# Kernel optimization log

Measured on AMD Instinct MI355X. Metric: run time of the kernel, lower is better.

The kernel has to match this reference:

```python
import math
import jax, jax.numpy as jnp
import numpy as np

B, L, D, H, V, R, NL = 4, 1024, 1024, 16, 50257, 4, 3
LORA_SCALE = 32.0 / R  # alpha / r
EPS = 1e-5
GELU_C = math.sqrt(2.0 / math.pi)


def gelu(x):
    return 0.5 * x * (1.0 + jnp.tanh(GELU_C * (x + 0.044715 * x ** 3)))


def layer_norm(x, w, b):
    u = x.mean(-1, keepdims=True)
    s = ((x - u) ** 2).mean(-1, keepdims=True)
    return w * (x - u) / jnp.sqrt(s + EPS) + b


def setup_inputs() -> dict:
    key = jax.random.key(0)
    ks = jax.random.split(key, 10)
    std = 0.02
    inp = {
        'input_ids': jax.random.randint(ks[0], (B, L), 0, V),
        'wte': jax.random.normal(ks[1], (V, D), jnp.float32) * std,
        'wpe': jax.random.normal(ks[2], (L, D), jnp.float32) * std,
        'ln1_w': jnp.ones((NL, D), jnp.float32),
        'ln1_b': jnp.zeros((NL, D), jnp.float32),
        'attn_w': jax.random.normal(ks[3], (NL, D, 3 * D), jnp.float32) * std,
        'attn_b': jnp.zeros((NL, 3 * D), jnp.float32),
        'lora_A': jax.random.normal(ks[4], (NL, 2 * R, D), jnp.float32) * std,
        'lora_B': jax.random.normal(ks[5], (NL, 2 * D, R), jnp.float32) * std,
        'proj_w': jax.random.normal(ks[6], (NL, D, D), jnp.float32) * std,
        'proj_b': jnp.zeros((NL, D), jnp.float32),
        'ln2_w': jnp.ones((NL, D), jnp.float32),
        'ln2_b': jnp.zeros((NL, D), jnp.float32),
        'fc_w': jax.random.normal(ks[7], (NL, D, 4 * D), jnp.float32) * std,
        'fc_b': jnp.zeros((NL, 4 * D), jnp.float32),
        'fc2_w': jax.random.normal(ks[8], (NL, 4 * D, D), jnp.float32) * std,
        'fc2_b': jnp.zeros((NL, D), jnp.float32),
    }
    return inp


def block(x, causal, p):
    (ln1w, ln1b, aw, ab, lA, lB, pw, pb, ln2w, ln2b, fw, fb, f2w, f2b) = p
    h = layer_norm(x, ln1w, ln1b)
    # LoRA-merged QKV: base GEMM + low-rank deltas on Q and V groups
    qkv = h @ aw + ab                     # [B,L,3D]
    after_A = h @ lA.T                    # [B,L,2R]
    dq = after_A[..., :R] @ lB[:D].T * LORA_SCALE   # [B,L,D]
    dv = after_A[..., R:] @ lB[D:].T * LORA_SCALE   # [B,L,D]
    q = qkv[..., :D] + dq
    k = qkv[..., D:2 * D]
    v = qkv[..., 2 * D:] + dv
    # split heads -> [B,H,L,hd]
    hd = D // H
    q = q.reshape(B, L, H, hd).transpose(0, 2, 1, 3)
    k = k.reshape(B, L, H, hd).transpose(0, 2, 1, 3)
    v = v.reshape(B, L, H, hd).transpose(0, 2, 1, 3)
    w = jnp.einsum('bhqd,bhkd->bhqk', q, k) / math.sqrt(hd)
    w = w * causal - 1e10 * (1.0 - causal)  # multiplicative causal mask trick
    w = jax.nn.softmax(w, axis=-1)
    a = jnp.einsum('bhqk,bhkd->bhqd', w, v)
    a = a.transpose(0, 2, 1, 3).reshape(B, L, D)
    a = a @ pw + pb
    x = x + a
    m = layer_norm(x, ln2w, ln2b)
    m = gelu(m @ fw + fb) @ f2w + f2b
    return x + m


def reference(input_ids, wte, wpe, ln1_w, ln1_b, attn_w, attn_b, lora_A, lora_B,
              proj_w, proj_b, ln2_w, ln2_b, fc_w, fc_b, fc2_w, fc2_b):
    pos = jnp.arange(L)
    x = wte[input_ids] + wpe[pos][None, :, :]   # [B,L,D]
    causal = jnp.tril(jnp.ones((L, L), x.dtype))
    for i in range(NL):
        p = (ln1_w[i], ln1_b[i], attn_w[i], attn_b[i], lora_A[i], lora_B[i],
             proj_w[i], proj_b[i], ln2_w[i], ln2_b[i], fc_w[i], fc_b[i],
             fc2_w[i], fc2_b[i])
        x = block(x, causal, p)
    return x
```

## Files before the change

kernel.cpp:

```cpp
#include <hip/hip_runtime.h>

typedef __bf16 bf16x8 __attribute__((ext_vector_type(8)));
typedef float f32x4 __attribute__((ext_vector_type(4)));
typedef unsigned short u16x8 __attribute__((ext_vector_type(8)));
typedef unsigned short u16x4 __attribute__((ext_vector_type(4)));

#define DEV static __device__ __forceinline__

DEV unsigned short f2bf(float f){
  unsigned int u = __builtin_bit_cast(unsigned int, f);
  u += 0x7fffu + ((u >> 16) & 1u);
  return (unsigned short)(u >> 16);
}
DEV float bf2f(unsigned short h){
  return __builtin_bit_cast(float, ((unsigned int)h) << 16);
}
DEV f32x4 bf4_to_f32(u16x4 h){
  f32x4 r = {bf2f(h[0]), bf2f(h[1]), bf2f(h[2]), bf2f(h[3])};
  return r;
}
DEV float gelu_f(float x){
  float z = 0.7978845608028654f * (x + 0.044715f * x * x * x);
  float e = __expf(2.0f * z);
  float th = 1.0f - 2.0f / (e + 1.0f);
  return 0.5f * x * (1.0f + th);
}

#define BAR() do{ asm volatile("" ::: "memory"); __builtin_amdgcn_s_barrier(); asm volatile("" ::: "memory"); }while(0)
#define LGKM0() asm volatile("s_waitcnt lgkmcnt(0)" ::: "memory")

__global__ __launch_bounds__(256)
void prep_weights(const float* __restrict__ attnw, const float* __restrict__ lorA,
                  const float* __restrict__ lorB, const float* __restrict__ projw,
                  const float* __restrict__ fcw, const float* __restrict__ fc2w,
                  unsigned short* __restrict__ WTA, unsigned short* __restrict__ WTP,
                  unsigned short* __restrict__ WTF, unsigned short* __restrict__ WTF2){
  __shared__ float tile[32][33];
  const int blk = blockIdx.x;
  const int layer = blk / 12288;
  const int r = blk % 12288;
  const float* in; unsigned short* out; int R, C, bx, by; bool lora;
  if (r < 3072){
    in = attnw + (size_t)layer*1024*3072; out = WTA + (size_t)layer*3072*1024;
    R = 1024; C = 3072; bx = r % 96; by = r / 96; lora = true;
  } else if (r < 4096){
    int rr = r - 3072;
    in = projw + (size_t)layer*1024*1024; out = WTP + (size_t)layer*1024*1024;
    R = 1024; C = 1024; bx = rr % 32; by = rr / 32; lora = false;
  } else if (r < 8192){
    int rr = r - 4096;
    in = fcw + (size_t)layer*1024*4096; out = WTF + (size_t)layer*4096*1024;
    R = 1024; C = 4096; bx = rr % 128; by = rr / 128; lora = false;
  } else {
    int rr = r - 8192;
    in = fc2w + (size_t)layer*4096*1024; out = WTF2 + (size_t)layer*1024*4096;
    R = 4096; C = 1024; bx = rr % 32; by = rr / 32; lora = false;
  }
  const int tx = threadIdx.x & 31, ty = threadIdx.x >> 5;
  const int r0 = by * 32, c0 = bx * 32;
  #pragma unroll
  for (int k = 0; k < 4; ++k)
    tile[ty + k*8][tx] = in[(size_t)(r0 + ty + k*8) * C + c0 + tx];
  float la0=0.f, la1=0.f, la2=0.f, la3=0.f;
  int seg = 0;
  if (lora){
    const float* lA = lorA + (size_t)layer*8192;
    seg = (c0 < 1024) ? 0 : ((c0 >= 2048) ? 2 : 1);
    if (seg != 1){
      const int kk = r0 + tx;
      const int rb = (seg == 0) ? 0 : 4;
      la0 = lA[(rb+0)*1024 + kk]; la1 = lA[(rb+1)*1024 + kk];
      la2 = lA[(rb+2)*1024 + kk]; la3 = lA[(rb+3)*1024 + kk];
    }
  }
  __syncthreads();
  const float* lB = lorB + (size_t)layer*8192;
  #pragma unroll
  for (int k = 0; k < 4; ++k){
    int rr = ty + k*8;
    int c = c0 + rr;
    float v = tile[tx][rr];
    if (lora && seg != 1){
      int lbrow = (seg == 0) ? c : (c - 1024);
      f32x4 lb = *(const f32x4*)(lB + (size_t)lbrow*4);
      v += 8.0f * (la0*lb[0] + la1*lb[1] + la2*lb[2] + la3*lb[3]);
    }
    if (lora && seg == 1) v *= 0.125f;
    out[(size_t)c * R + r0 + tx] = f2bf(v);
  }
}

DEV void ln_finish(f32x4 v, const float* __restrict__ wgt,
                   const float* __restrict__ bia, unsigned short* __restrict__ out,
                   int m, int t, float* red){
  float s  = v[0] + v[1] + v[2] + v[3];
  float ss = v[0]*v[0] + v[1]*v[1] + v[2]*v[2] + v[3]*v[3];
  #pragma unroll
  for (int off = 32; off >= 1; off >>= 1){
    s  += __shfl_xor(s, off);
    ss += __shfl_xor(ss, off);
  }
  if ((t & 63) == 0){ red[(t>>6)*2] = s; red[(t>>6)*2+1] = ss; }
  __syncthreads();
  float S  = red[0] + red[2] + red[4] + red[6];
  float SS = red[1] + red[3] + red[5] + red[7];
  float mean = S * (1.0f/1024.0f);
  float var  = SS * (1.0f/1024.0f) - mean*mean;
  float rstd = rsqrtf(var + 1e-5f);
  f32x4 wv = *(const f32x4*)(wgt + t*4);
  f32x4 bv = *(const f32x4*)(bia + t*4);
  u16x4 o;
  #pragma unroll
  for (int j = 0; j < 4; ++j) o[j] = f2bf(wv[j] * (v[j] - mean) * rstd + bv[j]);
  *(u16x4*)(out + (size_t)m * 1024 + t*4) = o;
}

__global__ __launch_bounds__(256)
void embed_ln(const int* __restrict__ ids, const float* __restrict__ wte,
              const float* __restrict__ wpe, const float* __restrict__ wgt,
              const float* __restrict__ bia, float* __restrict__ x,
              unsigned short* __restrict__ hb){
  __shared__ float red[8];
  const int m = blockIdx.x, t = threadIdx.x;
  const int id = ids[m], lpos = m & 1023;
  f32x4 a = *(const f32x4*)(wte + (size_t)id * 1024 + t*4);
  f32x4 p = *(const f32x4*)(wpe + (size_t)lpos * 1024 + t*4);
  f32x4 v = a + p;
  *(f32x4*)(x + (size_t)m * 1024 + t*4) = v;
  ln_finish(v, wgt, bia, hb, m, t, red);
}

__global__ __launch_bounds__(256)
void ln_kernel(const float* __restrict__ x, const float* __restrict__ wgt,
               const float* __restrict__ bia, unsigned short* __restrict__ out){
  __shared__ float red[8];
  const int m = blockIdx.x, t = threadIdx.x;
  f32x4 v = *(const f32x4*)(x + (size_t)m * 1024 + t*4);
  ln_finish(v, wgt, bia, out, m, t, red);
}

__global__ __launch_bounds__(256)
void reduce_ln(const unsigned short* __restrict__ P, const float* __restrict__ res,
               const float* __restrict__ bias, float* __restrict__ xout,
               const float* __restrict__ wgt, const float* __restrict__ bia,
               unsigned short* __restrict__ hb){
  __shared__ float red[8];
  const int m = blockIdx.x, t = threadIdx.x;
  const size_t off = (size_t)m*1024 + t*4;
  const size_t MN = (size_t)4096*1024;
  f32x4 v = bf4_to_f32(*(const u16x4*)(P + off));
  v += bf4_to_f32(*(const u16x4*)(P + MN + off));
  v += bf4_to_f32(*(const u16x4*)(P + 2*MN + off));
  v += bf4_to_f32(*(const u16x4*)(P + 3*MN + off));
  v += *(const f32x4*)(res + off);
  v += *(const f32x4*)(bias + t*4);
  *(f32x4*)(xout + off) = v;
  ln_finish(v, wgt, bia, hb, m, t, red);
}

__global__ __launch_bounds__(256)
void fc2_reduce(const unsigned short* __restrict__ P, const float* __restrict__ res,
                const float* __restrict__ bias, float* __restrict__ out){
  const int m = blockIdx.x, t = threadIdx.x;
  const size_t off = (size_t)m*1024 + t*4;
  const size_t MN = (size_t)4096*1024;
  f32x4 v = bf4_to_f32(*(const u16x4*)(P + off));
  v += bf4_to_f32(*(const u16x4*)(P + MN + off));
  v += bf4_to_f32(*(const u16x4*)(P + 2*MN + off));
  v += bf4_to_f32(*(const u16x4*)(P + 3*MN + off));
  v += *(const f32x4*)(res + off);
  v += *(const f32x4*)(bias + t*4);
  *(f32x4*)(out + off) = v;
}

__global__ __launch_bounds__(256)
void assemble_vt(const unsigned short* __restrict__ qkv,
                 unsigned short* __restrict__ Vto){
  __shared__ unsigned short vt[64 * 72];
  const int t = threadIdx.x;
  const int bh = blockIdx.y, b = bh >> 4, h = bh & 15;
  const int l0 = blockIdx.x * 64;
  {
    const int li = t >> 2, c0 = (t & 3) * 16;
    const unsigned short* src = qkv + (size_t)(b*1024 + l0 + li)*3072 + 2048 + h*64 + c0;
    u16x8 v0 = *(const u16x8*)(src);
    u16x8 v1 = *(const u16x8*)(src + 8);
    #pragma unroll
    for (int j = 0; j < 8; ++j){
      vt[(c0 + j)*72 + li]     = v0[j];
      vt[(c0 + 8 + j)*72 + li] = v1[j];
    }
  }
  __syncthreads();
  {
    const int dh = t >> 2, lc = (t & 3) * 16;
    u16x8 lo = *(const u16x8*)(&vt[dh*72 + lc]);
    u16x8 hi = *(const u16x8*)(&vt[dh*72 + lc + 8]);
    unsigned short* dst = Vto + ((size_t)(bh*64 + dh)) * 1024 + l0 + lc;
    *(u16x8*)(dst)     = lo;
    *(u16x8*)(dst + 8) = hi;
  }
}

template<int MODE>
__global__ __launch_bounds__(512, 1)
void gemm256(const unsigned short* __restrict__ A,
             const unsigned short* __restrict__ Wt,
             const float* __restrict__ bias,
             void* __restrict__ outp, int M, int N, int K, int ldk){
  extern __shared__ char sm[];
  const int t = threadIdx.x, w = t >> 6, l = t & 63, g = l >> 4, q = l & 15;
  const int wr = w >> 2, wc = w & 3;
  const int gx = gridDim.x;
  const int nwg = gx * gridDim.y;
  const int id  = blockIdx.x + gx * blockIdx.y;
  const int id2 = (id & 7) * (nwg >> 3) + (id >> 3);
  const int bm = (id2 / gx) * 256, bn = (id2 % gx) * 256;
  const int koff = blockIdx.z * K;
  const int NT = K >> 6;
  const int sr = t >> 3, sc = (t & 7) ^ (sr & 7);
  __attribute__((address_space(3))) char* smAS = (__attribute__((address_space(3))) char*)sm;

#define STAGE_A(slot, qd, tile) do{ \
    const unsigned short* _s = A + (size_t)(bm + (qd)*64 + sr)*ldk + koff + ((tile)<<6) + sc*8; \
    __builtin_amdgcn_global_load_lds((const __attribute__((address_space(1))) void*)_s, \
      (__attribute__((address_space(3))) void*)(smAS + (slot)*32768 + (qd)*8192 + t*16), 16, 0, 0); }while(0)
#define STAGE_B(slot, qd, tile) do{ \
    const unsigned short* _s = Wt + (size_t)(bn + (qd)*64 + sr)*ldk + koff + ((tile)<<6) + sc*8; \
    __builtin_amdgcn_global_load_lds((const __attribute__((address_space(1))) void*)_s, \
      (__attribute__((address_space(3))) void*)(smAS + 65536 + (slot)*32768 + (qd)*8192 + t*16), 16, 0, 0); }while(0)

  const int arow = (wr*128 + q) * 128;
  const int brow = (wc*64  + q) * 128;
  const int c0 = ((g    ) ^ (q & 7)) << 4;
  const int c1 = ((4 + g) ^ (q & 7)) << 4;

  f32x4 acc[8][4];
  #pragma unroll
  for (int m = 0; m < 8; ++m)
    #pragma unroll
    for (int n = 0; n < 4; ++n) acc[m][n] = (f32x4){0.f,0.f,0.f,0.f};

  STAGE_A(0,0,0); STAGE_A(0,1,0); STAGE_A(0,2,0); STAGE_A(0,3,0);
  STAGE_B(0,0,0); STAGE_B(0,1,0); STAGE_B(0,2,0); STAGE_B(0,3,0);
  if (NT > 1){
    STAGE_B(1,0,1); STAGE_B(1,1,1); STAGE_B(1,2,1); STAGE_B(1,3,1);
    STAGE_A(1,0,1); STAGE_A(1,2,1);
    asm volatile("s_waitcnt vmcnt(6)" ::: "memory");
  } else {
    asm volatile("s_waitcnt vmcnt(0)" ::: "memory");
  }
  BAR();

  u16x8 bk0[4], bk1[4];
  for (int T = 0; T < NT; ++T){
    const int cur = T & 1, nxt = cur ^ 1;
    const int curA = cur*32768, curB = 65536 + cur*32768;
    if (T + 1 < NT){ STAGE_A(nxt, 1, T+1); STAGE_A(nxt, 3, T+1); }
    u16x8 a00 = *(const u16x8*)(sm + curA + arow + 0*2048 + c0);
    u16x8 a01 = *(const u16x8*)(sm + curA + arow + 0*2048 + c1);
    u16x8 a10 = *(const u16x8*)(sm + curA + arow + 1*2048 + c0);
    u16x8 a11 = *(const u16x8*)(sm + curA + arow + 1*2048 + c1);
    #pragma unroll
    for (int n = 0; n < 4; ++n){
      bk0[n] = *(const u16x8*)(sm + curB + brow + n*2048 + c0);
      bk1[n] = *(const u16x8*)(sm + curB + brow + n*2048 + c1);
    }
    BAR(); LGKM0();
    __builtin_amdgcn_s_setprio(1);
    #pragma unroll
    for (int n = 0; n < 4; ++n){
      acc[0][n] = __builtin_amdgcn_mfma_f32_16x16x32_bf16(__builtin_bit_cast(bf16x8,a00), __builtin_bit_cast(bf16x8,bk0[n]), acc[0][n], 0,0,0);
      acc[0][n] = __builtin_amdgcn_mfma_f32_16x16x32_bf16(__builtin_bit_cast(bf16x8,a01), __builtin_bit_cast(bf16x8,bk1[n]), acc[0][n], 0,0,0);
      acc[1][n] = __builtin_amdgcn_mfma_f32_16x16x32_bf16(__builtin_bit_cast(bf16x8,a10), __builtin_bit_cast(bf16x8,bk0[n]), acc[1][n], 0,0,0);
      acc[1][n] = __builtin_amdgcn_mfma_f32_16x16x32_bf16(__builtin_bit_cast(bf16x8,a11), __builtin_bit_cast(bf16x8,bk1[n]), acc[1][n], 0,0,0);
    }
    __builtin_amdgcn_s_setprio(0);
    BAR();
    if (T + 2 < NT){ STAGE_B(cur, 0, T+2); STAGE_B(cur, 1, T+2); }
    a00 = *(const u16x8*)(sm + curA + arow + 2*2048 + c0);
    a01 = *(const u16x8*)(sm + curA + arow + 2*2048 + c1);
    a10 = *(const u16x8*)(sm + curA + arow + 3*2048 + c0);
    a11 = *(const u16x8*)(sm + curA + arow + 3*2048 + c1);
    BAR(); LGKM0();
    __builtin_amdgcn_s_setprio(1);
    #pragma unroll
    for (int n = 0; n < 4; ++n){
      acc[2][n] = __builtin_amdgcn_mfma_f32_16x16x32_bf16(__builtin_bit_cast(bf16x8,a00), __builtin_bit_cast(bf16x8,bk0[n]), acc[2][n], 0,0,0);
      acc[2][n] = __builtin_amdgcn_mfma_f32_16x16x32_bf16(__builtin_bit_cast(bf16x8,a01), __builtin_bit_cast(bf16x8,bk1[n]), acc[2][n], 0,0,0);
      acc[3][n] = __builtin_amdgcn_mfma_f32_16x16x32_bf16(__builtin_bit_cast(bf16x8,a10), __builtin_bit_cast(bf16x8,bk0[n]), acc[3][n], 0,0,0);
      acc[3][n] = __builtin_amdgcn_mfma_f32_16x16x32_bf16(__builtin_bit_cast(bf16x8,a11), __builtin_bit_cast(bf16x8,bk1[n]), acc[3][n], 0,0,0);
    }
    __builtin_amdgcn_s_setprio(0);
    BAR();
    if (T + 2 < NT){ STAGE_B(cur, 2, T+2); STAGE_B(cur, 3, T+2); STAGE_A(cur, 0, T+2); STAGE_A(cur, 2, T+2); }
    a00 = *(const u16x8*)(sm + curA + arow + 4*2048 + c0);
    a01 = *(const u16x8*)(sm + curA + arow + 4*2048 + c1);
    a10 = *(const u16x8*)(sm + curA + arow + 5*2048 + c0);
    a11 = *(const u16x8*)(sm + curA + arow + 5*2048 + c1);
    BAR(); LGKM0();
    __builtin_amdgcn_s_setprio(1);
    #pragma unroll
    for (int n = 0; n < 4; ++n){
      acc[4][n] = __builtin_amdgcn_mfma_f32_16x16x32_bf16(__builtin_bit_cast(bf16x8,a00), __builtin_bit_cast(bf16x8,bk0[n]), acc[4][n], 0,0,0);
      acc[4][n] = __builtin_amdgcn_mfma_f32_16x16x32_bf16(__builtin_bit_cast(bf16x8,a01), __builtin_bit_cast(bf16x8,bk1[n]), acc[4][n], 0,0,0);
      acc[5][n] = __builtin_amdgcn_mfma_f32_16x16x32_bf16(__builtin_bit_cast(bf16x8,a10), __builtin_bit_cast(bf16x8,bk0[n]), acc[5][n], 0,0,0);
      acc[5][n] = __builtin_amdgcn_mfma_f32_16x16x32_bf16(__builtin_bit_cast(bf16x8,a11), __builtin_bit_cast(bf16x8,bk1[n]), acc[5][n], 0,0,0);
    }
    __builtin_amdgcn_s_setprio(0);
    BAR();
    a00 = *(const u16x8*)(sm + curA + arow + 6*2048 + c0);
    a01 = *(const u16x8*)(sm + curA + arow + 6*2048 + c1);
    a10 = *(const u16x8*)(sm + curA + arow + 7*2048 + c0);
    a11 = *(const u16x8*)(sm + curA + arow + 7*2048 + c1);
    if (T + 2 < NT){ asm volatile("s_waitcnt vmcnt(6)" ::: "memory"); }
    else if (T + 1 < NT){ asm volatile("s_waitcnt vmcnt(0)" ::: "memory"); }
    BAR(); LGKM0();
    __builtin_amdgcn_s_setprio(1);
    #pragma unroll
    for (int n = 0; n < 4; ++n){
      acc[6][n] = __builtin_amdgcn_mfma_f32_16x16x32_bf16(__builtin_bit_cast(bf16x8,a00), __builtin_bit_cast(bf16x8,bk0[n]), acc[6][n], 0,0,0);
      acc[6][n] = __builtin_amdgcn_mfma_f32_16x16x32_bf16(__builtin_bit_cast(bf16x8,a01), __builtin_bit_cast(bf16x8,bk1[n]), acc[6][n], 0,0,0);
      acc[7][n] = __builtin_amdgcn_mfma_f32_16x16x32_bf16(__builtin_bit_cast(bf16x8,a10), __builtin_bit_cast(bf16x8,bk0[n]), acc[7][n], 0,0,0);
      acc[7][n] = __builtin_amdgcn_mfma_f32_16x16x32_bf16(__builtin_bit_cast(bf16x8,a11), __builtin_bit_cast(bf16x8,bk1[n]), acc[7][n], 0,0,0);
    }
    __builtin_amdgcn_s_setprio(0);
    BAR();
  }
#undef STAGE_A
#undef STAGE_B
  unsigned short* pout4 = (MODE == 4) ? ((unsigned short*)outp + (size_t)blockIdx.z * M * N) : nullptr;
  #pragma unroll
  for (int n = 0; n < 4; ++n){
    int col = bn + wc*64 + n*16 + q;
    float bv = (MODE == 4) ? 0.f : bias[col];
    if (MODE == 3 && (col >> 10) == 1) bv *= 0.125f;
    #pragma unroll
    for (int m = 0; m < 8; ++m){
      int row0 = bm + wr*128 + m*16 + g*4;
      #pragma unroll
      for (int r = 0; r < 4; ++r){
        float v = acc[m][n][r] + bv;
        if (MODE == 2){
          ((unsigned short*)outp)[(size_t)(row0 + r)*N + col] = f2bf(gelu_f(v));
        } else if (MODE == 3){
          ((unsigned short*)outp)[(size_t)(row0 + r)*N + col] = f2bf(v);
        } else if (MODE == 4){
          pout4[(size_t)(row0 + r)*N + col] = f2bf(v);
        }
      }
    }
  }
}

template<int MODE>
__global__ __launch_bounds__(256)
void gemm_bf16(const unsigned short* __restrict__ A,
               const unsigned short* __restrict__ Wt,
               const float* __restrict__ bias,
               const float* __restrict__ res,
               void* __restrict__ outp,
               int M, int N, int K){
  __shared__ unsigned short As[128*32];
  __shared__ unsigned short Bs[128*32];
  const int t = threadIdx.x;
  const int w = t >> 6, l = t & 63;
  const int wr = w >> 1, wc = w & 1;
  const int g = l >> 4, q = l & 15;
  const int gxn = gridDim.x;
  const int nwg = gxn * gridDim.y;
  const int bid = blockIdx.x + gxn * blockIdx.y;
  const int bid2 = ((nwg & 7) == 0) ? ((bid & 7)*(nwg >> 3) + (bid >> 3)) : bid;
  const int bm = (bid2 / gxn) * 128, bn = (bid2 % gxn) * 128;
  const int srow = t >> 2, schunk = t & 3;
  const unsigned short* Ag = A  + (size_t)(bm + srow)*K + schunk*8;
  const unsigned short* Bg = Wt + (size_t)(bn + srow)*K + schunk*8;
  const int sa0 = srow*64        + ((schunk ^ ((srow>>1)&3)) << 4);
  const int sa1 = (srow+64)*64   + ((schunk ^ (((srow+64)>>1)&3)) << 4);
  f32x4 acc[4][4];
  #pragma unroll
  for (int m = 0; m < 4; ++m)
    #pragma unroll
    for (int n = 0; n < 4; ++n) acc[m][n] = (f32x4){0.f,0.f,0.f,0.f};
  const int nk = K >> 5;
  u16x8 ra0 = *(const u16x8*)(Ag);
  u16x8 ra1 = *(const u16x8*)(Ag + (size_t)64*K);
  u16x8 rb0 = *(const u16x8*)(Bg);
  u16x8 rb1 = *(const u16x8*)(Bg + (size_t)64*K);
  for (int kt = 0; kt < nk; ++kt){
    __syncthreads();
    *(u16x8*)((char*)As + sa0) = ra0;
    *(u16x8*)((char*)As + sa1) = ra1;
    *(u16x8*)((char*)Bs + sa0) = rb0;
    *(u16x8*)((char*)Bs + sa1) = rb1;
    __syncthreads();
    if (kt + 1 < nk){
      const unsigned short* A2 = Ag + (size_t)(kt+1)*32;
      const unsigned short* B2 = Bg + (size_t)(kt+1)*32;
      ra0 = *(const u16x8*)(A2);
      ra1 = *(const u16x8*)(A2 + (size_t)64*K);
      rb0 = *(const u16x8*)(B2);
      rb1 = *(const u16x8*)(B2 + (size_t)64*K);
    }
    bf16x8 af[4], bfr[4];
    #pragma unroll
    for (int m = 0; m < 4; ++m){
      int row = wr*64 + m*16 + q;
      af[m] = __builtin_bit_cast(bf16x8,
        *(const u16x8*)((char*)As + row*64 + ((g ^ ((row>>1)&3)) << 4)));
    }
    #pragma unroll
    for (int n = 0; n < 4; ++n){
      int row = wc*64 + n*16 + q;
      bfr[n] = __builtin_bit_cast(bf16x8,
        *(const u16x8*)((char*)Bs + row*64 + ((g ^ ((row>>1)&3)) << 4)));
    }
    #pragma unroll
    for (int m = 0; m < 4; ++m)
      #pragma unroll
      for (int n = 0; n < 4; ++n)
        acc[m][n] = __builtin_amdgcn_mfma_f32_16x16x32_bf16(af[m], bfr[n], acc[m][n], 0, 0, 0);
  }
  #pragma unroll
  for (int n = 0; n < 4; ++n){
    int col = bn + wc*64 + n*16 + q;
    float bv = bias[col];
    #pragma unroll
    for (int m = 0; m < 4; ++m){
      int row0 = bm + wr*64 + m*16 + g*4;
      #pragma unroll
      for (int r = 0; r < 4; ++r){
        int row = row0 + r;
        float v = acc[m][n][r] + bv;
        if (MODE == 1) v += res[(size_t)row*N + col];
        if (MODE == 2){
          ((unsigned short*)outp)[(size_t)row*N + col] = f2bf(gelu_f(v));
        } else {
          ((float*)outp)[(size_t)row*N + col] = v;
        }
      }
    }
  }
}

__global__ __launch_bounds__(256)
void attn_kernel(const unsigned short* __restrict__ qkv,
                 const unsigned short* __restrict__ Vt,
                 unsigned short* __restrict__ Aout){
  __shared__ unsigned short Ks[64*64];
  __shared__ unsigned short Vs[64*64];
  const int t = threadIdx.x, w = t >> 6, l = t & 63, g = l >> 4, q = l & 15;
  const int qb = blockIdx.x, bh = blockIdx.y;
  const int b = bh >> 4, h = bh & 15;
  const size_t vbase = (size_t)bh * 65536;
  const int qrow = qb*64 + w*16 + q;
  const unsigned short* Qr = qkv + (size_t)(b*1024 + qrow)*3072 + h*64;
  bf16x8 qf0 = __builtin_bit_cast(bf16x8, *(const u16x8*)(Qr + g*8));
  bf16x8 qf1 = __builtin_bit_cast(bf16x8, *(const u16x8*)(Qr + 32 + g*8));
  f32x4 o[4];
  #pragma unroll
  for (int d = 0; d < 4; ++d) o[d] = (f32x4){0.f,0.f,0.f,0.f};
  float mprev = -1e30f, lsum = 0.f;
  const int srow = t >> 3, schunk = t & 7;
  const int nkt = qb + 1;
  u16x8 kvr[2], vvr[2];
  #pragma unroll
  for (int it = 0; it < 2; ++it){
    int r = srow + it*32;
    kvr[it] = *(const u16x8*)(qkv + (size_t)(b*1024 + r)*3072 + 1024 + h*64 + schunk*8);
    vvr[it] = *(const u16x8*)(Vt + vbase + (size_t)r*1024 + schunk*8);
  }
  for (int kt = 0; kt < nkt; ++kt){
    __syncthreads();
    #pragma unroll
    for (int it = 0; it < 2; ++it){
      int r = srow + it*32;
      *(u16x8*)((char*)Ks + r*128 + ((schunk ^ (r&7)) << 4)) = kvr[it];
      *(u16x8*)((char*)Vs + r*128 + ((schunk ^ (r&7)) << 4)) = vvr[it];
    }
    __syncthreads();
    if (kt + 1 < nkt){
      const int k1 = (kt + 1) * 64;
      #pragma unroll
      for (int it = 0; it < 2; ++it){
        int r = srow + it*32;
        kvr[it] = *(const u16x8*)(qkv + (size_t)(b*1024 + k1 + r)*3072 + 1024 + h*64 + schunk*8);
        vvr[it] = *(const u16x8*)(Vt + vbase + (size_t)r*1024 + k1 + schunk*8);
      }
    }
    const int k0 = kt * 64;
    f32x4 st[4];
    #pragma unroll
    for (int kf = 0; kf < 4; ++kf) st[kf] = (f32x4){0.f,0.f,0.f,0.f};
    #pragma unroll
    for (int kf = 0; kf < 4; ++kf){
      int krow = kf*16 + q;
      bf16x8 k0f = __builtin_bit_cast(bf16x8,
        *(const u16x8*)((char*)Ks + krow*128 + ((g       ^ (krow&7)) << 4)));
      bf16x8 k1f = __builtin_bit_cast(bf16x8,
        *(const u16x8*)((char*)Ks + krow*128 + (((4 + g) ^ (krow&7)) << 4)));
      st[kf] = __builtin_amdgcn_mfma_f32_16x16x32_bf16(k0f, qf0, st[kf], 0, 0, 0);
      st[kf] = __builtin_amdgcn_mfma_f32_16x16x32_bf16(k1f, qf1, st[kf], 0, 0, 0);
    }
    if (kt == nkt - 1){
      #pragma unroll
      for (int kf = 0; kf < 4; ++kf)
        #pragma unroll
        for (int r = 0; r < 4; ++r){
          int kg = k0 + kf*16 + g*4 + r;
          if (kg > qrow) st[kf][r] = -1e30f;
        }
    }
    float tmax = -1e30f;
    #pragma unroll
    for (int kf = 0; kf < 4; ++kf)
      #pragma unroll
      for (int r = 0; r < 4; ++r) tmax = fmaxf(tmax, st[kf][r]);
    tmax = fmaxf(tmax, __shfl_xor(tmax, 16));
    tmax = fmaxf(tmax, __shfl_xor(tmax, 32));
    float mnew = fmaxf(mprev, tmax);
    float p[4][4]; float tsum = 0.f;
    #pragma unroll
    for (int kf = 0; kf < 4; ++kf)
      #pragma unroll
      for (int r = 0; r < 4; ++r){
        float e = __expf(st[kf][r] - mnew);
        p[kf][r] = e; tsum += e;
      }
    tsum += __shfl_xor(tsum, 16);
    tsum += __shfl_xor(tsum, 32);
    float alpha = __expf(mprev - mnew);
    lsum = lsum * alpha + tsum;
    mprev = mnew;
    float al0 = __shfl(alpha, 20*g + 0);
    float al1 = __shfl(alpha, 20*g + 1);
    float al2 = __shfl(alpha, 20*g + 2);
    float al3 = __shfl(alpha, 20*g + 3);
    #pragma unroll
    for (int d = 0; d < 4; ++d){
      o[d][0] *= al0; o[d][1] *= al1; o[d][2] *= al2; o[d][3] *= al3;
    }
    #pragma unroll
    for (int ks = 0; ks < 2; ++ks){
      u16x8 pau;
      #pragma unroll
      for (int j = 0; j < 8; ++j){
        int gsel = (g & 1) ? (2 + (j >> 2)) : (j >> 2);
        int src = (gsel << 4) | q;
        float v0 = __shfl(p[2*ks + 0][j & 3], src);
        float v1 = __shfl(p[2*ks + 1][j & 3], src);
        pau[j] = f2bf((g >= 2) ? v1 : v0);
      }
      bf16x8 pa = __builtin_bit_cast(bf16x8, pau);
      #pragma unroll
      for (int df = 0; df < 4; ++df){
        int vrow = df*16 + q;
        bf16x8 vf = __builtin_bit_cast(bf16x8,
          *(const u16x8*)((char*)Vs + vrow*128 + (((ks*4 + g) ^ (vrow&7)) << 4)));
        o[df] = __builtin_amdgcn_mfma_f32_16x16x32_bf16(pa, vf, o[df], 0, 0, 0);
      }
    }
  }
  float r0 = 1.f / __shfl(lsum, 20*g + 0);
  float r1 = 1.f / __shfl(lsum, 20*g + 1);
  float r2 = 1.f / __shfl(lsum, 20*g + 2);
  float r3 = 1.f / __shfl(lsum, 20*g + 3);
  const int orow0 = qb*64 + w*16 + g*4;
  #pragma unroll
  for (int df = 0; df < 4; ++df){
    int col = h*64 + df*16 + q;
    Aout[((size_t)(b*1024 + orow0 + 0))*1024 + col] = f2bf(o[df][0] * r0);
    Aout[((size_t)(b*1024 + orow0 + 1))*1024 + col] = f2bf(o[df][1] * r1);
    Aout[((size_t)(b*1024 + orow0 + 2))*1024 + col] = f2bf(o[df][2] * r2);
    Aout[((size_t)(b*1024 + orow0 + 3))*1024 + col] = f2bf(o[df][3] * r3);
  }
}

extern "C" void kernel_launch(void* const* d_in, const int* in_sizes, int n_in,
                              void* d_out, int out_size, void* d_ws, size_t ws_size,
                              hipStream_t stream){
  (void)in_sizes; (void)n_in; (void)out_size; (void)ws_size;
  const int*   ids   = (const int*)  d_in[0];
  const float* wte   = (const float*)d_in[1];
  const float* wpe   = (const float*)d_in[2];
  const float* ln1w  = (const float*)d_in[3];
  const float* ln1b  = (const float*)d_in[4];
  const float* attnw = (const float*)d_in[5];
  const float* attnb = (const float*)d_in[6];
  const float* lorA  = (const float*)d_in[7];
  const float* lorB  = (const float*)d_in[8];
  const float* projw = (const float*)d_in[9];
  const float* projb = (const float*)d_in[10];
  const float* ln2w  = (const float*)d_in[11];
  const float* ln2b  = (const float*)d_in[12];
  const float* fcw   = (const float*)d_in[13];
  const float* fcb   = (const float*)d_in[14];
  const float* fc2w  = (const float*)d_in[15];
  const float* fc2b  = (const float*)d_in[16];

  char* p = (char*)d_ws;
  float* XA  = (float*)p;                    p += 16777216;
  float* XB  = (float*)p;                    p += 16777216;
  unsigned short* HB   = (unsigned short*)p; p += 8388608;
  unsigned short* MBf  = (unsigned short*)p; p += 8388608;
  unsigned short* QKVb = (unsigned short*)p; p += 25165824;
  unsigned short* Vtb  = (unsigned short*)p; p += 8388608;
  unsigned short* AO   = (unsigned short*)p; p += 8388608;
  unsigned short* ACT  = (unsigned short*)p; p += 33554432;
  unsigned short* PSUM = (unsigned short*)p; p += 33554432;
  unsigned short* WTA  = (unsigned short*)p; p += 18874368;
  unsigned short* WTP  = (unsigned short*)p; p += 6291456;
  unsigned short* WTF  = (unsigned short*)p; p += 25165824;
  unsigned short* WTF2 = (unsigned short*)p; p += 25165824;

  prep_weights<<<36864, 256, 0, stream>>>(attnw, lorA, lorB, projw, fcw, fc2w,
                                          WTA, WTP, WTF, WTF2);
  embed_ln<<<4096, 256, 0, stream>>>(ids, wte, wpe, ln1w, ln1b, XA, HB);

  for (int i = 0; i < 3; ++i){
    gemm256<3><<<dim3(12, 16), 512, 131072, stream>>>(HB, WTA + (size_t)i*3072*1024, attnb + i*3072, QKVb, 4096, 3072, 1024, 1024);
    assemble_vt<<<dim3(16, 64), 256, 0, stream>>>(QKVb, Vtb);
    attn_kernel<<<dim3(16, 64), 256, 0, stream>>>(QKVb, Vtb, AO);
    gemm_bf16<1><<<dim3(8, 32), 256, 0, stream>>>(AO, WTP + (size_t)i*1024*1024, projb + i*1024, XA, XB, 4096, 1024, 1024);
    ln_kernel<<<4096, 256, 0, stream>>>(XB, ln2w + i*1024, ln2b + i*1024, MBf);
    gemm256<2><<<dim3(16, 16), 512, 131072, stream>>>(MBf, WTF + (size_t)i*4096*1024, fcb + i*4096, ACT, 4096, 4096, 1024, 1024);
    gemm256<4><<<dim3(4, 16, 4), 512, 131072, stream>>>(ACT, WTF2 + (size_t)i*1024*4096, nullptr, PSUM, 4096, 1024, 1024, 4096);
    if (i < 2){
      reduce_ln<<<4096, 256, 0, stream>>>(PSUM, XB, fc2b + i*1024, XA,
                                          ln1w + (i+1)*1024, ln1b + (i+1)*1024, HB);
    } else {
      fc2_reduce<<<4096, 256, 0, stream>>>(PSUM, XB, fc2b + i*1024, (float*)d_out);
    }
  }
}
```

Before: 715.0 us.

## Fuse V transpose into QKV GEMM epilogue and streamline weight prep and softmax packing

The QKV GEMM gets a new epilogue mode that writes the V columns straight into the transposed per-head layout, so the separate assemble_vt kernel and its extra pass over V are dropped. The weight-prep kernel now folds in the LoRA delta during the load phase and writes transposed bf16 output with vectorized 4-element stores. Attention packs probabilities into bf16 pairs before the cross-lane shuffles, halving the shuffle count. f2bf now uses the hardware bf16 conversion. The V epilogue writes strided 8-byte chunks, which may coalesce less well than the row-major stores.

```diff
diff --git a/kernel.cpp b/kernel.cpp
--- a/kernel.cpp
+++ b/kernel.cpp
@@ -4,13 +4,12 @@
 typedef float f32x4 __attribute__((ext_vector_type(4)));
 typedef unsigned short u16x8 __attribute__((ext_vector_type(8)));
 typedef unsigned short u16x4 __attribute__((ext_vector_type(4)));
+typedef unsigned int u32x4 __attribute__((ext_vector_type(4)));
 
 #define DEV static __device__ __forceinline__
 
 DEV unsigned short f2bf(float f){
-  unsigned int u = __builtin_bit_cast(unsigned int, f);
-  u += 0x7fffu + ((u >> 16) & 1u);
-  return (unsigned short)(u >> 16);
+  return __builtin_bit_cast(unsigned short, (__bf16)f);
 }
 DEV float bf2f(unsigned short h){
   return __builtin_bit_cast(float, ((unsigned int)h) << 16);
@@ -56,38 +55,38 @@
     in = fc2w + (size_t)layer*4096*1024; out = WTF2 + (size_t)layer*1024*4096;
     R = 4096; C = 1024; bx = rr % 32; by = rr / 32; lora = false;
   }
-  const int tx = threadIdx.x & 31, ty = threadIdx.x >> 5;
+  const int t = threadIdx.x;
+  const int tx = t & 31, ty = t >> 5;
   const int r0 = by * 32, c0 = bx * 32;
-  #pragma unroll
-  for (int k = 0; k < 4; ++k)
-    tile[ty + k*8][tx] = in[(size_t)(r0 + ty + k*8) * C + c0 + tx];
-  float la0=0.f, la1=0.f, la2=0.f, la3=0.f;
   int seg = 0;
+  f32x4 lb = {0.f, 0.f, 0.f, 0.f};
+  const float* lA = nullptr;
   if (lora){
-    const float* lA = lorA + (size_t)layer*8192;
     seg = (c0 < 1024) ? 0 : ((c0 >= 2048) ? 2 : 1);
     if (seg != 1){
-      const int kk = r0 + tx;
-      const int rb = (seg == 0) ? 0 : 4;
-      la0 = lA[(rb+0)*1024 + kk]; la1 = lA[(rb+1)*1024 + kk];
-      la2 = lA[(rb+2)*1024 + kk]; la3 = lA[(rb+3)*1024 + kk];
-    }
+      int c = c0 + tx;
+      int lbrow = (seg == 0) ? c : (c - 1024);
+      lb = *(const f32x4*)(lorB + (size_t)layer*8192 + (size_t)lbrow*4);
+      lA = lorA + (size_t)layer*8192 + ((seg == 0) ? 0 : 4096);
+    }
+  }
+  #pragma unroll
+  for (int kk = 0; kk < 4; ++kk){
+    int krow = r0 + ty + kk*8;
+    float v = in[(size_t)krow * C + c0 + tx];
+    if (lora && seg != 1){
+      v += 8.0f * (lA[krow]*lb[0] + lA[1024 + krow]*lb[1] +
+                   lA[2048 + krow]*lb[2] + lA[3072 + krow]*lb[3]);
+    }
+    if (lora && seg == 1) v *= 0.125f;
+    tile[ty + kk*8][tx] = v;
   }
   __syncthreads();
-  const float* lB = lorB + (size_t)layer*8192;
-  #pragma unroll
-  for (int k = 0; k < 4; ++k){
-    int rr = ty + k*8;
-    int c = c0 + rr;
-    float v = tile[tx][rr];
-    if (lora && seg != 1){
-      int lbrow = (seg == 0) ? c : (c - 1024);
-      f32x4 lb = *(const f32x4*)(lB + (size_t)lbrow*4);
-      v += 8.0f * (la0*lb[0] + la1*lb[1] + la2*lb[2] + la3*lb[3]);
-    }
-    if (lora && seg == 1) v *= 0.125f;
-    out[(size_t)c * R + r0 + tx] = f2bf(v);
-  }
+  const int orow = t >> 3, oc4 = (t & 7) * 4;
+  u16x4 ov;
+  #pragma unroll
+  for (int c = 0; c < 4; ++c) ov[c] = f2bf(tile[oc4 + c][orow]);
+  *(u16x4*)(out + (size_t)(c0 + orow) * R + r0 + oc4) = ov;
 }
 
 DEV void ln_finish(f32x4 v, const float* __restrict__ wgt,
@@ -173,41 +172,13 @@
   *(f32x4*)(out + off) = v;
 }
 
-__global__ __launch_bounds__(256)
-void assemble_vt(const unsigned short* __restrict__ qkv,
-                 unsigned short* __restrict__ Vto){
-  __shared__ unsigned short vt[64 * 72];
-  const int t = threadIdx.x;
-  const int bh = blockIdx.y, b = bh >> 4, h = bh & 15;
-  const int l0 = blockIdx.x * 64;
-  {
-    const int li = t >> 2, c0 = (t & 3) * 16;
-    const unsigned short* src = qkv + (size_t)(b*1024 + l0 + li)*3072 + 2048 + h*64 + c0;
-    u16x8 v0 = *(const u16x8*)(src);
-    u16x8 v1 = *(const u16x8*)(src + 8);
-    #pragma unroll
-    for (int j = 0; j < 8; ++j){
-      vt[(c0 + j)*72 + li]     = v0[j];
-      vt[(c0 + 8 + j)*72 + li] = v1[j];
-    }
-  }
-  __syncthreads();
-  {
-    const int dh = t >> 2, lc = (t & 3) * 16;
-    u16x8 lo = *(const u16x8*)(&vt[dh*72 + lc]);
-    u16x8 hi = *(const u16x8*)(&vt[dh*72 + lc + 8]);
-    unsigned short* dst = Vto + ((size_t)(bh*64 + dh)) * 1024 + l0 + lc;
-    *(u16x8*)(dst)     = lo;
-    *(u16x8*)(dst + 8) = hi;
-  }
-}
-
 template<int MODE>
 __global__ __launch_bounds__(512, 1)
 void gemm256(const unsigned short* __restrict__ A,
              const unsigned short* __restrict__ Wt,
              const float* __restrict__ bias,
-             void* __restrict__ outp, int M, int N, int K, int ldk){
+             void* __restrict__ outp, void* __restrict__ outp2,
+             int M, int N, int K, int ldk){
   extern __shared__ char sm[];
   const int t = threadIdx.x, w = t >> 6, l = t & 63, g = l >> 4, q = l & 15;
   const int wr = w >> 2, wc = w & 3;
@@ -334,19 +305,28 @@
   for (int n = 0; n < 4; ++n){
     int col = bn + wc*64 + n*16 + q;
     float bv = (MODE == 4) ? 0.f : bias[col];
-    if (MODE == 3 && (col >> 10) == 1) bv *= 0.125f;
+    if (MODE == 5 && (col >> 10) == 1) bv *= 0.125f;
     #pragma unroll
     for (int m = 0; m < 8; ++m){
       int row0 = bm + wr*128 + m*16 + g*4;
-      #pragma unroll
-      for (int r = 0; r < 4; ++r){
-        float v = acc[m][n][r] + bv;
-        if (MODE == 2){
-          ((unsigned short*)outp)[(size_t)(row0 + r)*N + col] = f2bf(gelu_f(v));
-        } else if (MODE == 3){
-          ((unsigned short*)outp)[(size_t)(row0 + r)*N + col] = f2bf(v);
-        } else if (MODE == 4){
-          pout4[(size_t)(row0 + r)*N + col] = f2bf(v);
+      if (MODE == 5 && col >= 2048){
+        int dh = col & 63, hh = (col >> 6) & 15;
+        int bb = row0 >> 10, ll = row0 & 1023;
+        u16x4 pv;
+        #pragma unroll
+        for (int r = 0; r < 4; ++r) pv[r] = f2bf(acc[m][n][r] + bv);
+        *(u16x4*)((unsigned short*)outp2 + ((size_t)(bb*16 + hh)*64 + dh)*1024 + ll) = pv;
+      } else {
+        #pragma unroll
+        for (int r = 0; r < 4; ++r){
+          float v = acc[m][n][r] + bv;
+          if (MODE == 2){
+            ((unsigned short*)outp)[(size_t)(row0 + r)*N + col] = f2bf(gelu_f(v));
+          } else if (MODE == 5){
+            ((unsigned short*)outp)[(size_t)(row0 + r)*N + col] = f2bf(v);
+          } else if (MODE == 4){
+            pout4[(size_t)(row0 + r)*N + col] = f2bf(v);
+          }
         }
       }
     }
@@ -540,18 +520,28 @@
     for (int d = 0; d < 4; ++d){
       o[d][0] *= al0; o[d][1] *= al1; o[d][2] *= al2; o[d][3] *= al3;
     }
+    unsigned pk0[4], pk1[4];
+    #pragma unroll
+    for (int kf = 0; kf < 4; ++kf){
+      pk0[kf] = (unsigned)f2bf(p[kf][0]) | ((unsigned)f2bf(p[kf][1]) << 16);
+      pk1[kf] = (unsigned)f2bf(p[kf][2]) | ((unsigned)f2bf(p[kf][3]) << 16);
+    }
+    const int sa = (((g & 1) << 1) << 4) | q;
+    const int sb = ((((g & 1) << 1) | 1) << 4) | q;
+    const bool hi2 = (g >= 2);
     #pragma unroll
     for (int ks = 0; ks < 2; ++ks){
-      u16x8 pau;
-      #pragma unroll
-      for (int j = 0; j < 8; ++j){
-        int gsel = (g & 1) ? (2 + (j >> 2)) : (j >> 2);
-        int src = (gsel << 4) | q;
-        float v0 = __shfl(p[2*ks + 0][j & 3], src);
-        float v1 = __shfl(p[2*ks + 1][j & 3], src);
-        pau[j] = f2bf((g >= 2) ? v1 : v0);
-      }
-      bf16x8 pa = __builtin_bit_cast(bf16x8, pau);
+      const int kA = 2*ks, kB = 2*ks + 1;
+      unsigned a0 = (unsigned)__shfl((int)pk0[kA], sa);
+      unsigned b0 = (unsigned)__shfl((int)pk0[kB], sa);
+      unsigned a1 = (unsigned)__shfl((int)pk1[kA], sa);
+      unsigned b1 = (unsigned)__shfl((int)pk1[kB], sa);
+      unsigned a2 = (unsigned)__shfl((int)pk0[kA], sb);
+      unsigned b2 = (unsigned)__shfl((int)pk0[kB], sb);
+      unsigned a3 = (unsigned)__shfl((int)pk1[kA], sb);
+      unsigned b3 = (unsigned)__shfl((int)pk1[kB], sb);
+      u32x4 pw = { hi2 ? b0 : a0, hi2 ? b1 : a1, hi2 ? b2 : a2, hi2 ? b3 : a3 };
+      bf16x8 pa = __builtin_bit_cast(bf16x8, pw);
       #pragma unroll
       for (int df = 0; df < 4; ++df){
         int vrow = df*16 + q;
@@ -618,13 +608,12 @@
   embed_ln<<<4096, 256, 0, stream>>>(ids, wte, wpe, ln1w, ln1b, XA, HB);
 
   for (int i = 0; i < 3; ++i){
-    gemm256<3><<<dim3(12, 16), 512, 131072, stream>>>(HB, WTA + (size_t)i*3072*1024, attnb + i*3072, QKVb, 4096, 3072, 1024, 1024);
-    assemble_vt<<<dim3(16, 64), 256, 0, stream>>>(QKVb, Vtb);
+    gemm256<5><<<dim3(12, 16), 512, 131072, stream>>>(HB, WTA + (size_t)i*3072*1024, attnb + i*3072, QKVb, Vtb, 4096, 3072, 1024, 1024);
     attn_kernel<<<dim3(16, 64), 256, 0, stream>>>(QKVb, Vtb, AO);
     gemm_bf16<1><<<dim3(8, 32), 256, 0, stream>>>(AO, WTP + (size_t)i*1024*1024, projb + i*1024, XA, XB, 4096, 1024, 1024);
     ln_kernel<<<4096, 256, 0, stream>>>(XB, ln2w + i*1024, ln2b + i*1024, MBf);
-    gemm256<2><<<dim3(16, 16), 512, 131072, stream>>>(MBf, WTF + (size_t)i*4096*1024, fcb + i*4096, ACT, 4096, 4096, 1024, 1024);
-    gemm256<4><<<dim3(4, 16, 4), 512, 131072, stream>>>(ACT, WTF2 + (size_t)i*1024*4096, nullptr, PSUM, 4096, 1024, 1024, 4096);
+    gemm256<2><<<dim3(16, 16), 512, 131072, stream>>>(MBf, WTF + (size_t)i*4096*1024, fcb + i*4096, ACT, nullptr, 4096, 4096, 1024, 1024);
+    gemm256<4><<<dim3(4, 16, 4), 512, 131072, stream>>>(ACT, WTF2 + (size_t)i*1024*4096, nullptr, PSUM, nullptr, 4096, 1024, 1024, 4096);
     if (i < 2){
       reduce_ln<<<4096, 256, 0, stream>>>(PSUM, XB, fc2b + i*1024, XA,
                                           ln1w + (i+1)*1024, ln1b + (i+1)*1024, HB);
```

Measured after the change: 681.9 us. 1.05x faster.
